# Optimization experiments

Hardware: AMD Instinct MI355X
Metric: run time of the kernel (lower is better)

The kernel has to match this reference:

```python
import jax, jax.numpy as jnp
import numpy as np

B, S, E, H = 2, 2048, 1024, 16
D = E // H  # head_dim = 64


def setup_inputs() -> dict:
    key = jax.random.key(0)
    k1, k2, k3 = jax.random.split(key, 3)
    scale_in = 1.0 / np.sqrt(E)
    return {
        "x": jax.random.normal(k1, (B, S, E), dtype=jnp.float32),
        "mask": jnp.ones((B, S), dtype=jnp.int32),
        "qkv_w": jax.random.normal(k2, (3 * E, E), dtype=jnp.float32) * scale_in,
        "qkv_b": jnp.zeros((3 * E,), dtype=jnp.float32),
        "proj_w": jax.random.normal(k3, (E, E), dtype=jnp.float32) * scale_in,
        "proj_b": jnp.zeros((E,), dtype=jnp.float32),
    }


def reference(x, mask, qkv_w, qkv_b, proj_w, proj_b):
    b, s, e = x.shape
    # fused QKV projection: torch Linear -> x @ W^T + b
    qkv = x @ qkv_w.T + qkv_b                      # [B,S,3E]
    qkv = qkv.reshape(b, s, 3, H, D).transpose(2, 0, 3, 1, 4)  # [3,B,H,S,D]
    q, k, v = qkv[0], qkv[1], qkv[2]
    scores = jnp.einsum("bhqd,bhkd->bhqk", q, k) / jnp.sqrt(jnp.float32(D))
    # mask [B,S] -> [B,1,1,S]; masked_fill(mask==0, -inf)
    m = mask[:, None, None, :]
    scores = jnp.where(m == 0, -jnp.inf, scores)
    attn = jax.nn.softmax(scores, axis=-1)
    attn = jnp.nan_to_num(attn, nan=0.0)           # fully-masked rows -> 0
    # dropout is identity in eval mode (deterministic reference)
    out = jnp.einsum("bhqk,bhkd->bhqd", attn, v)   # [B,H,S,D]
    out = out.transpose(0, 2, 1, 3).reshape(b, s, e)
    out = out @ proj_w.T + proj_b
    return out
```

## Files before the change

kernel.cpp:

```cpp
#include <hip/hip_runtime.h>
#include <hip/hip_bf16.h>

#define B_ 2
#define S_ 2048
#define E_ 1024
#define H_ 16
#define D_ 64

typedef __bf16 bf16x8 __attribute__((ext_vector_type(8)));
typedef __bf16 bf16x4 __attribute__((ext_vector_type(4)));
typedef float f32x4 __attribute__((ext_vector_type(4)));


__device__ __forceinline__ f32x4 mfma16(bf16x8 a, bf16x8 b, f32x4 c) {
    return __builtin_amdgcn_mfma_f32_16x16x32_bf16(a, b, c, 0, 0, 0);
}

__device__ __forceinline__ void gl_lds16(const __bf16* g, __bf16* l) {
    __builtin_amdgcn_global_load_lds(
        (const __attribute__((address_space(1))) unsigned int*)g,
        (__attribute__((address_space(3))) unsigned int*)l, 16, 0, 0);
}
__device__ __forceinline__ void gl_lds4(const int* g, int* l) {
    __builtin_amdgcn_global_load_lds(
        (const __attribute__((address_space(1))) unsigned int*)g,
        (__attribute__((address_space(3))) unsigned int*)l, 4, 0, 0);
}

__global__ __launch_bounds__(256) void convert_kernel(
        const float* __restrict__ x, const float* __restrict__ qkvw,
        const float* __restrict__ projw, __bf16* __restrict__ ws) {
    const long NX = 4194304, NW = 3145728;
    long i = (long)(blockIdx.x * 256 + threadIdx.x) * 4;
    const float* src; __bf16* dst; long off;
    if (i < NX)           { src = x;     dst = ws;           off = i; }
    else if (i < NX + NW) { src = qkvw;  dst = ws + NX;      off = i - NX; }
    else                  { src = projw; dst = ws + NX + NW; off = i - NX - NW; }
    float4 v = *(const float4*)(src + off);
    bf16x4 o = { (__bf16)v.x, (__bf16)v.y, (__bf16)v.z, (__bf16)v.w };
    *(bf16x4*)(dst + off) = o;
}

__device__ __forceinline__ void gemm_core(
        const __bf16* __restrict__ A, const __bf16* __restrict__ Bm,
        int rowT, int colT, int K,
        __bf16* AT, __bf16* BT, f32x4 acc[4][4]) {
    int tid = threadIdx.x;
    int wave = tid >> 6, lane = tid & 63;
    int quad = lane >> 4, lm = lane & 15;
    int wy = wave >> 1, wx = wave & 1;
    int srow = wave * 8 + (lane >> 3);
    int schunk = lane & 7;
    const __bf16* ap = A + (long)(rowT + srow) * K + schunk * 8;
    const __bf16* bp = Bm + (long)(colT + srow) * K + schunk * 8;
    for (int k0 = 0; k0 < K; k0 += 64) {
        __syncthreads();
        for (int i = 0; i < 4; i++) {
            gl_lds16(ap + (long)i * 32 * K + k0, AT + (i * 256 + wave * 64) * 8);
            gl_lds16(bp + (long)i * 32 * K + k0, BT + (i * 256 + wave * 64) * 8);
        }
        __syncthreads();
        for (int ks = 0; ks < 2; ks++) {
            bf16x8 af[4], bfr[4];
            for (int m = 0; m < 4; m++)
                af[m] = *(const bf16x8*)(AT + (wy * 64 + m * 16 + lm) * 64 + ks * 32 + quad * 8);
            for (int n = 0; n < 4; n++)
                bfr[n] = *(const bf16x8*)(BT + (wx * 64 + n * 16 + lm) * 64 + ks * 32 + quad * 8);
            for (int m = 0; m < 4; m++)
                for (int n = 0; n < 4; n++)
                    acc[m][n] = mfma16(af[m], bfr[n], acc[m][n]);
        }
    }
}

__device__ __forceinline__ void gemm_core_h(
        const __bf16* __restrict__ A, const __bf16* __restrict__ Bm,
        int rowT, int colT, int K,
        __bf16* AT, __bf16* BT, f32x4 acc[2][4]) {
    int tid = threadIdx.x;
    int wave = tid >> 6, lane = tid & 63;
    int quad = lane >> 4, lm = lane & 15;
    int srow = wave * 8 + (lane >> 3);
    int schunk = lane & 7;
    const __bf16* ap = A + (long)(rowT + srow) * K + schunk * 8;
    const __bf16* bp = Bm + (long)(colT + srow) * K + schunk * 8;
    for (int k0 = 0; k0 < K; k0 += 64) {
        __syncthreads();
        for (int i = 0; i < 4; i++)
            gl_lds16(ap + (long)i * 32 * K + k0, AT + (i * 256 + wave * 64) * 8);
        for (int i = 0; i < 2; i++)
            gl_lds16(bp + (long)i * 32 * K + k0, BT + (i * 256 + wave * 64) * 8);
        __syncthreads();
        for (int ks = 0; ks < 2; ks++) {
            bf16x8 af[2], bfr[4];
            for (int m = 0; m < 2; m++)
                af[m] = *(const bf16x8*)(AT + (wave * 32 + m * 16 + lm) * 64 + ks * 32 + quad * 8);
            for (int n = 0; n < 4; n++)
                bfr[n] = *(const bf16x8*)(BT + (n * 16 + lm) * 64 + ks * 32 + quad * 8);
            for (int m = 0; m < 2; m++)
                for (int n = 0; n < 4; n++)
                    acc[m][n] = mfma16(af[m], bfr[n], acc[m][n]);
        }
    }
}

#define C1 0.18033688011112043f

__global__ __launch_bounds__(256, 3) void qkv_gemm(
        const __bf16* __restrict__ xbf, const __bf16* __restrict__ wbf,
        const float* __restrict__ bias, __bf16* __restrict__ qk,
        __bf16* __restrict__ vt) {
    __shared__ __align__(16) __bf16 AT[128 * 64];
    __shared__ __align__(16) __bf16 BT[128 * 64];
    f32x4 acc[4][4] = {};
    int rowT = blockIdx.x * 128, colT = blockIdx.y * 128;
    gemm_core(xbf, wbf, rowT, colT, E_, AT, BT, acc);
    int wave = threadIdx.x >> 6, lane = threadIdx.x & 63;
    int quad = lane >> 4, lm = lane & 15;
    int wy = wave >> 1, wx = wave & 1;
    int which = colT >> 10;
    if (which < 2) {
        float sc = which ? 1.f : C1;
        for (int n = 0; n < 4; n++) {
            int col = colT + wx * 64 + n * 16 + lm;
            float bv = bias[col];
            int rem = col & 1023;
            int h = rem >> 6, d = rem & 63;
            for (int m = 0; m < 4; m++) {
                int rowb = rowT + wy * 64 + m * 16 + quad * 4;
                for (int r = 0; r < 4; r++) {
                    int row = rowb + r;
                    int b = row >> 11, s = row & 2047;
                    float v = (acc[m][n][r] + bv) * sc;
                    qk[(long)((which * B_ + b) * H_ + h) * (S_ * D_) + (long)s * D_ + d] = (__bf16)v;
                }
            }
        }
    } else {
        for (int n = 0; n < 4; n++) {
            int col = colT + wx * 64 + n * 16 + lm;
            float bv = bias[col];
            int mr = col & 1023;
            int h = mr >> 6, d = mr & 63;
            for (int m = 0; m < 4; m++) {
                int row = rowT + wy * 64 + m * 16 + quad * 4;
                int b = row >> 11, s = row & 2047;
                bf16x4 o = { (__bf16)(acc[m][n][0] + bv), (__bf16)(acc[m][n][1] + bv),
                             (__bf16)(acc[m][n][2] + bv), (__bf16)(acc[m][n][3] + bv) };
                *(bf16x4*)(vt + (long)((b * H_ + h) * D_ + d) * S_ + s) = o;
            }
        }
    }
}

__global__ __launch_bounds__(512, 2) void flash_attn(
        const __bf16* __restrict__ qk, const __bf16* __restrict__ vt,
        const int* __restrict__ mask, __bf16* __restrict__ attn) {
    int wave = threadIdx.x >> 6, lane = threadIdx.x & 63;
    int quad = lane >> 4, lm = lane & 15;
    int bh = blockIdx.x;
    int qb = blockIdx.y;
    int b = bh >> 4, h = bh & 15;
    const long BHSD = (long)B_ * H_ * S_ * D_;
    const __bf16* qp  = qk + (long)bh * (S_ * D_);
    const __bf16* kp  = qk + BHSD + (long)bh * (S_ * D_);
    const __bf16* vtp = vt + (long)bh * (D_ * S_);
    const int* mrow = mask + b * S_;

    __shared__ __align__(16) __bf16 Kl[2][128 * 64];
    __shared__ __align__(16) __bf16 Vl[2][64 * 128];
    __shared__ __align__(16) int    Ml[2][128];
    __shared__ __align__(16) __bf16 Plds[8][2][16][136];

    int q0[2];
    q0[0] = qb * 256 + wave * 32;
    q0[1] = q0[0] + 16;
    bf16x8 qa[2][2];
    for (int t = 0; t < 2; t++)
        for (int x = 0; x < 2; x++)
            qa[t][x] = *(const bf16x8*)(qp + (long)(q0[t] + lm) * D_ + x * 32 + quad * 8);

    f32x4 O[2][4] = {};
    f32x4 Ol[2] = {};
    bf16x8 ones8;
    for (int j = 0; j < 8; j++) ones8[j] = (__bf16)1.0f;

    struct __align__(8) bfx4 { __hip_bfloat162 lo, hi; };

    int r8 = lane >> 3, c8 = lane & 7;
    int cs = c8 ^ r8;
    int xs = lm & 7;

    {
        #pragma unroll
        for (int j = 0; j < 2; j++) {
            int wp = wave * 2 + j;
            int krow = wp * 8 + r8;
            gl_lds16(kp + (long)krow * 64 + cs * 8, &Kl[0][wp * 512]);
            int vrow = wp * 4 + quad;
            int vcs = lm ^ (vrow & 15);
            gl_lds16(vtp + (long)vrow * S_ + vcs * 8, &Vl[0][wp * 512]);
        }
        if (wave == 0) {
            gl_lds4(mrow + lane, &Ml[0][0]);
            gl_lds4(mrow + 64 + lane, &Ml[0][64]);
        }
    }
    __syncthreads();

    for (int i = 0; i < 16; i++) {
        int bs = i & 1;
        if (i < 15) {
            int kb1 = (i + 1) * 128;
            #pragma unroll
            for (int j = 0; j < 2; j++) {
                int wp = wave * 2 + j;
                int krow = wp * 8 + r8;
                gl_lds16(kp + (long)(kb1 + krow) * 64 + cs * 8, &Kl[bs ^ 1][wp * 512]);
                int vrow = wp * 4 + quad;
                int vcs = lm ^ (vrow & 15);
                gl_lds16(vtp + (long)vrow * S_ + kb1 + vcs * 8, &Vl[bs ^ 1][wp * 512]);
            }
            if (wave == 0) {
                gl_lds4(mrow + kb1 + lane, &Ml[bs ^ 1][0]);
                gl_lds4(mrow + kb1 + 64 + lane, &Ml[bs ^ 1][64]);
            }
        }
        const __bf16* Kb = &Kl[bs][0];
        #pragma unroll
        for (int g = 0; g < 4; g++) {
            bf16x8 kf[2][2];
            f32x4 zsel[2];
            #pragma unroll
            for (int j = 0; j < 2; j++) {
                int hh = g * 2 + j;
                int row = hh * 16 + lm;
                kf[j][0] = *(const bf16x8*)(Kb + row * 64 + ((quad ^ xs) << 3));
                kf[j][1] = *(const bf16x8*)(Kb + row * 64 + (((4 + quad) ^ xs) << 3));
                int4 mq = *(const int4*)(&Ml[bs][hh * 16 + quad * 4]);
                zsel[j][0] = mq.x ? -32.f : -1e38f;
                zsel[j][1] = mq.y ? -32.f : -1e38f;
                zsel[j][2] = mq.z ? -32.f : -1e38f;
                zsel[j][3] = mq.w ? -32.f : -1e38f;
            }
            f32x4 st[2][2];
            __builtin_amdgcn_s_setprio(1);
            #pragma unroll
            for (int j = 0; j < 2; j++)
                #pragma unroll
                for (int t = 0; t < 2; t++) {
                    f32x4 z = mfma16(kf[j][0], qa[t][0], zsel[j]);
                    st[j][t] = mfma16(kf[j][1], qa[t][1], z);
                }
            __builtin_amdgcn_s_setprio(0);
            #pragma unroll
            for (int j = 0; j < 2; j++)
                #pragma unroll
                for (int t = 0; t < 2; t++) {
                    int hh = g * 2 + j;
                    float e0 = __builtin_amdgcn_exp2f(st[j][t][0]);
                    float e1 = __builtin_amdgcn_exp2f(st[j][t][1]);
                    float e2 = __builtin_amdgcn_exp2f(st[j][t][2]);
                    float e3 = __builtin_amdgcn_exp2f(st[j][t][3]);
                    bfx4 pk;
                    pk.lo = __float22bfloat162_rn(float2{e0, e1});
                    pk.hi = __float22bfloat162_rn(float2{e2, e3});
                    *(bfx4*)(&Plds[wave][t][lm][hh * 16 + quad * 4]) = pk;
                }
        }
        const __bf16* Vb = &Vl[bs][0];
        #pragma unroll
        for (int x = 0; x < 4; x++) {
            bf16x8 vf[4];
            #pragma unroll
            for (int c = 0; c < 4; c++) {
                int row = c * 16 + lm;
                vf[c] = *(const bf16x8*)(Vb + row * 128 + (((x * 4 + quad) ^ lm) << 3));
            }
            bf16x8 pa[2];
            #pragma unroll
            for (int t = 0; t < 2; t++)
                pa[t] = *(const bf16x8*)(&Plds[wave][t][lm][x * 32 + quad * 8]);
            __builtin_amdgcn_s_setprio(1);
            #pragma unroll
            for (int t = 0; t < 2; t++) {
                #pragma unroll
                for (int c = 0; c < 4; c++)
                    O[t][c] = mfma16(pa[t], vf[c], O[t][c]);
                Ol[t] = mfma16(pa[t], ones8, Ol[t]);
            }
            __builtin_amdgcn_s_setprio(0);
        }
        __syncthreads();
    }

    for (int t = 0; t < 2; t++)
        for (int r = 0; r < 4; r++) {
            float lb = Ol[t][r];
            float inv = lb > 0.f ? 1.f / lb : 0.f;
            int s = q0[t] + quad * 4 + r;
            for (int c = 0; c < 4; c++) {
                int e = h * 64 + c * 16 + lm;
                attn[(long)(b * S_ + s) * E_ + e] = (__bf16)(O[t][c][r] * inv);
            }
        }
}

__global__ __launch_bounds__(256, 2) void proj_gemm(
        const __bf16* __restrict__ abf, const __bf16* __restrict__ wbf,
        const float* __restrict__ bias, float* __restrict__ out) {
    __shared__ __align__(16) __bf16 AT[128 * 64];
    __shared__ __align__(16) __bf16 BT[64 * 64];
    f32x4 acc[2][4] = {};
    int rowT = blockIdx.x * 128, colT = blockIdx.y * 64;
    gemm_core_h(abf, wbf, rowT, colT, E_, AT, BT, acc);
    int wave = threadIdx.x >> 6, lane = threadIdx.x & 63;
    int quad = lane >> 4, lm = lane & 15;
    for (int n = 0; n < 4; n++) {
        int col = colT + n * 16 + lm;
        float bv = bias[col];
        for (int m = 0; m < 2; m++) {
            int rowb = rowT + wave * 32 + m * 16 + quad * 4;
            for (int r = 0; r < 4; r++) {
                int row = rowb + r;
                out[(long)row * E_ + col] = acc[m][n][r] + bv;
            }
        }
    }
}

extern "C" void kernel_launch(void* const* d_in, const int* in_sizes, int n_in,
                              void* d_out, int out_size, void* d_ws, size_t ws_size,
                              hipStream_t stream) {
    const float* x      = (const float*)d_in[0];
    const int*   mask   = (const int*)d_in[1];
    const float* qkv_w  = (const float*)d_in[2];
    const float* qkv_b  = (const float*)d_in[3];
    const float* proj_w = (const float*)d_in[4];
    const float* proj_b = (const float*)d_in[5];
    float* out = (float*)d_out;
    __bf16* ws = (__bf16*)d_ws;

    __bf16* x_bf     = ws;
    __bf16* qkvw_bf  = ws + 4194304;
    __bf16* projw_bf = ws + 7340032;
    __bf16* qk_bf    = ws + 8388608;
    __bf16* vt_bf    = ws + 16777216;
    __bf16* attn_bf  = ws + 20971520;

    convert_kernel<<<8192, 256, 0, stream>>>(x, qkv_w, proj_w, ws);
    qkv_gemm<<<dim3(32, 24), 256, 0, stream>>>(x_bf, qkvw_bf, qkv_b, qk_bf, vt_bf);
    flash_attn<<<dim3(32, 8), 512, 0, stream>>>(qk_bf, vt_bf, mask, attn_bf);
    proj_gemm<<<dim3(32, 16), 256, 0, stream>>>(attn_bf, projw_bf, proj_b, out);
}
```

Before: 185.5 us.

## Rewrite QKV GEMM with 256x256 tiles, triple-buffered LDS pipeline and swizzle

After: 188.2 us. No clear change (+1.5%).

```diff
diff --git a/kernel.cpp b/kernel.cpp
--- a/kernel.cpp
+++ b/kernel.cpp
@@ -39,38 +39,6 @@
     float4 v = *(const float4*)(src + off);
     bf16x4 o = { (__bf16)v.x, (__bf16)v.y, (__bf16)v.z, (__bf16)v.w };
     *(bf16x4*)(dst + off) = o;
-}
-
-__device__ __forceinline__ void gemm_core(
-        const __bf16* __restrict__ A, const __bf16* __restrict__ Bm,
-        int rowT, int colT, int K,
-        __bf16* AT, __bf16* BT, f32x4 acc[4][4]) {
-    int tid = threadIdx.x;
-    int wave = tid >> 6, lane = tid & 63;
-    int quad = lane >> 4, lm = lane & 15;
-    int wy = wave >> 1, wx = wave & 1;
-    int srow = wave * 8 + (lane >> 3);
-    int schunk = lane & 7;
-    const __bf16* ap = A + (long)(rowT + srow) * K + schunk * 8;
-    const __bf16* bp = Bm + (long)(colT + srow) * K + schunk * 8;
-    for (int k0 = 0; k0 < K; k0 += 64) {
-        __syncthreads();
-        for (int i = 0; i < 4; i++) {
-            gl_lds16(ap + (long)i * 32 * K + k0, AT + (i * 256 + wave * 64) * 8);
-            gl_lds16(bp + (long)i * 32 * K + k0, BT + (i * 256 + wave * 64) * 8);
-        }
-        __syncthreads();
-        for (int ks = 0; ks < 2; ks++) {
-            bf16x8 af[4], bfr[4];
-            for (int m = 0; m < 4; m++)
-                af[m] = *(const bf16x8*)(AT + (wy * 64 + m * 16 + lm) * 64 + ks * 32 + quad * 8);
-            for (int n = 0; n < 4; n++)
-                bfr[n] = *(const bf16x8*)(BT + (wx * 64 + n * 16 + lm) * 64 + ks * 32 + quad * 8);
-            for (int m = 0; m < 4; m++)
-                for (int n = 0; n < 4; n++)
-                    acc[m][n] = mfma16(af[m], bfr[n], acc[m][n]);
-        }
-    }
 }
 
 __device__ __forceinline__ void gemm_core_h(
@@ -106,28 +74,80 @@
 
 #define C1 0.18033688011112043f
 
-__global__ __launch_bounds__(256, 3) void qkv_gemm(
+__global__ __launch_bounds__(512, 2) void qkv_gemm(
         const __bf16* __restrict__ xbf, const __bf16* __restrict__ wbf,
         const float* __restrict__ bias, __bf16* __restrict__ qk,
         __bf16* __restrict__ vt) {
-    __shared__ __align__(16) __bf16 AT[128 * 64];
-    __shared__ __align__(16) __bf16 BT[128 * 64];
-    f32x4 acc[4][4] = {};
-    int rowT = blockIdx.x * 128, colT = blockIdx.y * 128;
-    gemm_core(xbf, wbf, rowT, colT, E_, AT, BT, acc);
-    int wave = threadIdx.x >> 6, lane = threadIdx.x & 63;
+    __shared__ __align__(16) __bf16 Ab[3][256 * 32];
+    __shared__ __align__(16) __bf16 Bb[3][256 * 32];
+    int tid = threadIdx.x;
+    int wave = tid >> 6, lane = tid & 63;
     int quad = lane >> 4, lm = lane & 15;
-    int wy = wave >> 1, wx = wave & 1;
+    int wr = wave >> 2, wc = wave & 3;
+    int rowT = blockIdx.x * 256, colT = blockIdx.y * 256;
+    int r16 = lane >> 2, c4 = lane & 3;
+    int cs = c4 ^ ((r16 >> 1) & 3);
+    const __bf16* asrc = xbf + (long)(rowT + wave * 32 + r16) * E_ + cs * 8;
+    const __bf16* bsrc = wbf + (long)(colT + wave * 32 + r16) * E_ + cs * 8;
+    int xr = quad ^ ((lm >> 1) & 3);
+
+    f32x4 acc[8][4] = {};
+
+#define STAGE_QKV(buf, k0) { \
+    gl_lds16(asrc + (k0),           &Ab[buf][(wave * 32) * 32]); \
+    gl_lds16(asrc + 16 * E_ + (k0), &Ab[buf][(wave * 32 + 16) * 32]); \
+    gl_lds16(bsrc + (k0),           &Bb[buf][(wave * 32) * 32]); \
+    gl_lds16(bsrc + 16 * E_ + (k0), &Bb[buf][(wave * 32 + 16) * 32]); }
+
+    STAGE_QKV(0, 0)
+    STAGE_QKV(1, 32)
+    asm volatile("s_waitcnt vmcnt(4)" ::: "memory");
+    __builtin_amdgcn_sched_barrier(0);
+    __builtin_amdgcn_s_barrier();
+    __builtin_amdgcn_sched_barrier(0);
+
+    #pragma unroll
+    for (int k = 0; k < 32; k++) {
+        const int cur = k % 3;
+        bf16x8 a[8], bfr[4];
+        #pragma unroll
+        for (int m = 0; m < 8; m++)
+            a[m] = *(const bf16x8*)(&Ab[cur][(wr * 128 + m * 16 + lm) * 32 + xr * 8]);
+        #pragma unroll
+        for (int n = 0; n < 4; n++)
+            bfr[n] = *(const bf16x8*)(&Bb[cur][(wc * 64 + n * 16 + lm) * 32 + xr * 8]);
+        asm volatile("s_waitcnt lgkmcnt(0)" ::: "memory");
+        __builtin_amdgcn_sched_barrier(0);
+        __builtin_amdgcn_s_barrier();
+        __builtin_amdgcn_sched_barrier(0);
+        if (k < 30) STAGE_QKV((k + 2) % 3, (k + 2) * 32)
+        __builtin_amdgcn_s_setprio(1);
+        #pragma unroll
+        for (int m = 0; m < 8; m++)
+            #pragma unroll
+            for (int n = 0; n < 4; n++)
+                acc[m][n] = mfma16(a[m], bfr[n], acc[m][n]);
+        __builtin_amdgcn_s_setprio(0);
+        if (k < 30) { asm volatile("s_waitcnt vmcnt(4)" ::: "memory"); }
+        else        { asm volatile("s_waitcnt vmcnt(0)" ::: "memory"); }
+        __builtin_amdgcn_sched_barrier(0);
+        __builtin_amdgcn_s_barrier();
+        __builtin_amdgcn_sched_barrier(0);
+    }
+#undef STAGE_QKV
+
     int which = colT >> 10;
     if (which < 2) {
         float sc = which ? 1.f : C1;
+        #pragma unroll
         for (int n = 0; n < 4; n++) {
-            int col = colT + wx * 64 + n * 16 + lm;
+            int col = colT + wc * 64 + n * 16 + lm;
             float bv = bias[col];
             int rem = col & 1023;
             int h = rem >> 6, d = rem & 63;
-            for (int m = 0; m < 4; m++) {
-                int rowb = rowT + wy * 64 + m * 16 + quad * 4;
+            #pragma unroll
+            for (int m = 0; m < 8; m++) {
+                int rowb = rowT + wr * 128 + m * 16 + quad * 4;
                 for (int r = 0; r < 4; r++) {
                     int row = rowb + r;
                     int b = row >> 11, s = row & 2047;
@@ -137,13 +157,15 @@
             }
         }
     } else {
+        #pragma unroll
         for (int n = 0; n < 4; n++) {
-            int col = colT + wx * 64 + n * 16 + lm;
+            int col = colT + wc * 64 + n * 16 + lm;
             float bv = bias[col];
             int mr = col & 1023;
             int h = mr >> 6, d = mr & 63;
-            for (int m = 0; m < 4; m++) {
-                int row = rowT + wy * 64 + m * 16 + quad * 4;
+            #pragma unroll
+            for (int m = 0; m < 8; m++) {
+                int row = rowT + wr * 128 + m * 16 + quad * 4;
                 int b = row >> 11, s = row & 2047;
                 bf16x4 o = { (__bf16)(acc[m][n][0] + bv), (__bf16)(acc[m][n][1] + bv),
                              (__bf16)(acc[m][n][2] + bv), (__bf16)(acc[m][n][3] + bv) };
@@ -349,7 +371,7 @@
     __bf16* attn_bf  = ws + 20971520;
 
     convert_kernel<<<8192, 256, 0, stream>>>(x, qkv_w, proj_w, ws);
-    qkv_gemm<<<dim3(32, 24), 256, 0, stream>>>(x_bf, qkvw_bf, qkv_b, qk_bf, vt_bf);
+    qkv_gemm<<<dim3(16, 12), 512, 0, stream>>>(x_bf, qkvw_bf, qkv_b, qk_bf, vt_bf);
     flash_attn<<<dim3(32, 8), 512, 0, stream>>>(qk_bf, vt_bf, mask, attn_bf);
     proj_gemm<<<dim3(32, 16), 256, 0, stream>>>(attn_bf, projw_bf, proj_b, out);
 }
```
